# Performance work log

Hardware: AMD Instinct MI355X
Metric: run time of the kernel (lower is better)

Reference implementation:

```python
import jax, jax.numpy as jnp
import numpy as np

N_AGENTS = 3
OBS_DIM = 30
ACT_DIM = 9
HIDDEN = 128
HEADS = 4
HEAD_DIM = HIDDEN // HEADS
BATCH = 131072
NEG_SLOPE = 0.01
MASK_VAL = -1e10


def _leaky(x):
    return jnp.where(x >= 0, x, NEG_SLOPE * x)


def setup_inputs() -> dict:
    key = jax.random.key(0)
    ks = jax.random.split(key, 20)

    def init(k, shape, fan_in):
        return jax.random.normal(k, shape, dtype=jnp.float32) / np.sqrt(fan_in)

    inp = {
        "observations": jax.random.normal(ks[0], (BATCH, N_AGENTS, OBS_DIM), dtype=jnp.float32),
        "actions": jax.random.uniform(ks[1], (BATCH, N_AGENTS, ACT_DIM), dtype=jnp.float32),
        # per-agent embed weights, stacked over agents: [N, in, out] (already transposed vs torch)
        "W_o": init(ks[2], (N_AGENTS, OBS_DIM, HIDDEN), OBS_DIM),
        "b_o": jnp.zeros((N_AGENTS, HIDDEN), dtype=jnp.float32),
        "W_oa": init(ks[3], (N_AGENTS, OBS_DIM + ACT_DIM, HIDDEN), OBS_DIM + ACT_DIM),
        "b_oa": jnp.zeros((N_AGENTS, HIDDEN), dtype=jnp.float32),
        # shared attention projections: [in, out]
        "Wq": init(ks[4], (HIDDEN, HIDDEN), HIDDEN),
        "bq": jnp.zeros((HIDDEN,), dtype=jnp.float32),
        "Wk": init(ks[5], (HIDDEN, HIDDEN), HIDDEN),
        "bk": jnp.zeros((HIDDEN,), dtype=jnp.float32),
        "Wv": init(ks[6], (HIDDEN, HIDDEN), HIDDEN),
        "bv": jnp.zeros((HIDDEN,), dtype=jnp.float32),
        # per-agent critic MLP: Linear(2H->H) + LeakyReLU + Linear(H->A)
        "Wc1": init(ks[7], (N_AGENTS, 2 * HIDDEN, HIDDEN), 2 * HIDDEN),
        "bc1": jnp.zeros((N_AGENTS, HIDDEN), dtype=jnp.float32),
        "Wc2": init(ks[8], (N_AGENTS, HIDDEN, ACT_DIM), HIDDEN),
        "bc2": jnp.zeros((N_AGENTS, ACT_DIM), dtype=jnp.float32),
    }
    return inp


def reference(observations, actions, W_o, b_o, W_oa, b_oa, Wq, bq, Wk, bk, Wv, bv, Wc1, bc1, Wc2, bc2):
    B, N, _ = observations.shape

    # per-agent embeds as a single batched GEMM over the agent axis
    o_emb = _leaky(jnp.einsum('bnd,ndh->bnh', observations, W_o) + b_o)          # [B,N,H]
    oa = jnp.concatenate([observations, actions], axis=-1)                        # [B,N,O+A]
    oa_emb = _leaky(jnp.einsum('bnd,ndh->bnh', oa, W_oa) + b_oa)                  # [B,N,H]

    # shared Q/K/V projections, split heads -> [B, heads, N, head_dim]
    def heads(x):
        return x.reshape(B, N, HEADS, HEAD_DIM).transpose(0, 2, 1, 3)

    Q = heads(o_emb @ Wq + bq)
    K = heads(oa_emb @ Wk + bk)
    V = heads(oa_emb @ Wv + bv)

    scores = jnp.einsum('bhnd,bhmd->bhnm', Q, K) / np.sqrt(HEAD_DIM).astype(np.float32)
    mask = jnp.where(jnp.eye(N, dtype=bool), jnp.float32(MASK_VAL), 0.0)          # diag masked
    attn = jax.nn.softmax(scores + mask, axis=-1)
    attn_out = jnp.einsum('bhnm,bhmd->bhnd', attn, V)
    attn_out = attn_out.transpose(0, 2, 1, 3).reshape(B, N, HIDDEN)               # [B,N,H]

    # per-agent critics, again batched over the agent axis
    c_in = jnp.concatenate([o_emb, attn_out], axis=-1)                            # [B,N,2H]
    h = _leaky(jnp.einsum('bnd,ndh->bnh', c_in, Wc1) + bc1)
    q_values = jnp.einsum('bnh,nha->bna', h, Wc2) + bc2                           # [B,N,A]
    return q_values
```

## Files before the change

kernel.cpp:

```cpp
#include <hip/hip_runtime.h>
#include <stdint.h>

typedef unsigned short u16;
typedef unsigned int u32;
typedef __attribute__((ext_vector_type(8))) short short8;
typedef __attribute__((ext_vector_type(4))) float floatx4;

#define BATCH   131072
#define NA      3
#define OBS     30
#define ACTD    9
#define HID     128
#define HEADS   4
#define HD      32
#define MB      16
#define ROWS    (MB*NA)
#define LDC     136
#define LDOA    72
#define QSCALE  0.17677669529663687f

#define OFF_WO    0
#define OFF_WOA   12288
#define OFF_WQ    36864
#define OFF_WK    53248
#define OFF_WV    69632
#define OFF_WC1   86016
#define OFF_WC2   184320
#define PRE_TOTAL 190464

__device__ __forceinline__ u16 f2bf(float f) {
    union { float f; u32 u; } v; v.f = f;
    return (u16)((v.u + 0x8000u) >> 16);
}
__device__ __forceinline__ u32 pk_bf16(float a, float b) {
    union { float f; u32 u; } x, y; x.f = a; y.f = b;
    return ((x.u + 0x8000u) >> 16) | ((y.u + 0x8000u) & 0xffff0000u);
}
__device__ __forceinline__ float lo16f(u32 w) { union { u32 u; float f; } v; v.u = w << 16; return v.f; }
__device__ __forceinline__ float hi16f(u32 w) { union { u32 u; float f; } v; v.u = w & 0xffff0000u; return v.f; }
__device__ __forceinline__ float leaky(float x) { return x >= 0.f ? x : 0.01f * x; }

__global__ void prepack_kernel(const float* __restrict__ Wo,  const float* __restrict__ Woa,
                               const float* __restrict__ Wq,  const float* __restrict__ Wk,
                               const float* __restrict__ Wv,  const float* __restrict__ Wc1,
                               const float* __restrict__ Wc2, u16* __restrict__ out) {
    int i = blockIdx.x * blockDim.x + threadIdx.x;
    if (i >= PRE_TOTAL) return;
    const float* src; int K, KT, perA, base, Nsrc, Nlim; float scl = 1.f;
    if (i < OFF_WOA)      { src = Wo;  K = 30;  KT = 1; perA = 4096;  base = OFF_WO;  Nsrc = 128; Nlim = 128; }
    else if (i < OFF_WQ)  { src = Woa; K = 39;  KT = 2; perA = 8192;  base = OFF_WOA; Nsrc = 128; Nlim = 128; }
    else if (i < OFF_WK)  { src = Wq;  K = 128; KT = 4; perA = 16384; base = OFF_WQ;  Nsrc = 128; Nlim = 128; scl = QSCALE; }
    else if (i < OFF_WV)  { src = Wk;  K = 128; KT = 4; perA = 16384; base = OFF_WK;  Nsrc = 128; Nlim = 128; }
    else if (i < OFF_WC1) { src = Wv;  K = 128; KT = 4; perA = 16384; base = OFF_WV;  Nsrc = 128; Nlim = 128; }
    else if (i < OFF_WC2) { src = Wc1; K = 256; KT = 8; perA = 32768; base = OFF_WC1; Nsrc = 128; Nlim = 128; }
    else                  { src = Wc2; K = 128; KT = 4; perA = 2048;  base = OFF_WC2; Nsrc = 9;   Nlim = 9;   }
    int j = i - base;
    int agent = j / perA;
    int r = j - agent * perA;
    int e = r & 7, lane = (r >> 3) & 63, fk = r >> 9;
    int kt = fk % KT, nt = fk / KT;
    int n = nt * 16 + (lane & 15);
    int k = kt * 32 + (lane >> 4) * 8 + e;
    u16 v = 0;
    if (k < K && n < Nlim) v = f2bf(src[(agent * K + k) * Nsrc + n] * scl);
    out[i] = v;
}

__global__ __launch_bounds__(256, 3) void fused_kernel(
    const float* __restrict__ obs, const float* __restrict__ act,
    const float* __restrict__ b_o, const float* __restrict__ b_oa,
    const float* __restrict__ bq,  const float* __restrict__ bk_, const float* __restrict__ bv,
    const float* __restrict__ bc1, const float* __restrict__ bc2,
    const u16* __restrict__ pre, float* __restrict__ out)
{
    __shared__ __align__(16) u16 s_mem[4 * ROWS * LDC];
    __shared__ float2 s_probs[MB * HEADS * NA];
    u16* s_oemb  = s_mem;
    u16* s_oaemb = s_mem + ROWS * LDC;
    u16* s_bufA  = s_mem + 2 * ROWS * LDC;
    u16* s_bufB  = s_mem + 3 * ROWS * LDC;

    const int tid  = threadIdx.x;
    const int wave = tid >> 6, lane = tid & 63;
    const int l15  = lane & 15, quad = lane >> 4;
    const int b0   = blockIdx.x * MB;
    const short8* preV = (const short8*)pre;

    for (int g = tid; g < ROWS * 15; g += 256) {
        int r = g / 15, s = g - r * 15;
        int n = r / MB, bl = r - n * MB;
        const float* src = &obs[((b0 + bl) * NA + n) * OBS + 2 * s];
        *(u32*)&s_bufA[n * (MB * LDOA) + bl * LDOA + 2 * s] = pk_bf16(src[0], src[1]);
    }
    for (int g = tid; g < ROWS * 5; g += 256) {
        int r = g / 5, s = g - r * 5;
        int n = r / MB, bl = r - n * MB;
        const float* src = &act[((b0 + bl) * NA + n) * ACTD + 2 * s];
        float v0 = src[0], v1 = (s < 4) ? src[1] : 0.f;
        *(u32*)&s_bufA[n * (MB * LDOA) + bl * LDOA + 30 + 2 * s] = pk_bf16(v0, v1);
    }
    for (int g = tid; g < ROWS * 12; g += 256) {
        int r = g / 12, s = g - r * 12;
        int n = r / MB, bl = r - n * MB;
        *(u32*)&s_bufA[n * (MB * LDOA) + bl * LDOA + 40 + 2 * s] = 0;
    }
    __syncthreads();

    for (int sj = wave; sj < 12; sj += 4) {
        int osel = sj / 6;
        int rem = sj % 6, agent = rem >> 1, nh = rem & 1;
        int KTn = osel ? 2 : 1;
        const float* bias = osel ? b_oa : b_o;
        int preBase = osel ? (OFF_WOA / 8 + agent * 1024) : (OFF_WO / 8 + agent * 512);
        floatx4 acc[4] = {};
        for (int kt = 0; kt < KTn; kt++) {
            short8 a = *(const short8*)&s_bufA[agent * (MB * LDOA) + l15 * LDOA + kt * 32 + quad * 8];
            for (int n4 = 0; n4 < 4; n4++) {
                int nt = nh * 4 + n4;
                short8 b = preV[preBase + (nt * KTn + kt) * 64 + lane];
                acc[n4] = __builtin_amdgcn_mfma_f32_16x16x32_bf16(a, b, acc[n4], 0, 0, 0);
            }
        }
        u16* dst = osel ? s_oaemb : s_oemb;
        for (int n4 = 0; n4 < 4; n4++) {
            int col = (nh * 4 + n4) * 16 + l15;
            float bb = bias[agent * HID + col];
            for (int rg = 0; rg < 4; rg++) {
                int m = quad * 4 + rg;
                dst[(m * NA + agent) * LDC + col] = f2bf(leaky(acc[n4][rg] + bb));
            }
        }
    }
    __syncthreads();

    for (int sj = wave; sj < 12; sj += 4) {
        int proj = sj / 6;
        int rem = sj % 6, mt = rem >> 1, nh = rem & 1;
        const u16* A = proj ? s_oaemb : s_oemb;
        int preBase = (proj ? OFF_WK : OFF_WQ) / 8;
        const float* bias = proj ? bk_ : bq;
        float bscl = proj ? 1.f : QSCALE;
        floatx4 acc[4] = {};
        for (int kt = 0; kt < 4; kt++) {
            short8 a = *(const short8*)&A[(mt * 16 + l15) * LDC + kt * 32 + quad * 8];
            for (int n4 = 0; n4 < 4; n4++) {
                int nt = nh * 4 + n4;
                short8 b = preV[preBase + (nt * 4 + kt) * 64 + lane];
                acc[n4] = __builtin_amdgcn_mfma_f32_16x16x32_bf16(a, b, acc[n4], 0, 0, 0);
            }
        }
        u16* dst = proj ? s_bufB : s_bufA;
        for (int n4 = 0; n4 < 4; n4++) {
            int col = (nh * 4 + n4) * 16 + l15;
            float bb = bias[col] * bscl;
            for (int rg = 0; rg < 4; rg++) {
                int m = mt * 16 + quad * 4 + rg;
                dst[m * LDC + col] = f2bf(acc[n4][rg] + bb);
            }
        }
    }
    __syncthreads();

    if (tid < MB * HEADS * NA) {
        int e = tid / (HEADS * NA), r = tid - e * HEADS * NA, h = r / NA, n = r - h * NA;
        int m0 = (n == 0) ? 1 : 0;
        int m1 = (n == 2) ? 1 : 2;
        const uint4* qp = (const uint4*)&s_bufA[(e * NA + n) * LDC + h * HD];
        const uint4* kp0 = (const uint4*)&s_bufB[(e * NA + m0) * LDC + h * HD];
        const uint4* kp1 = (const uint4*)&s_bufB[(e * NA + m1) * LDC + h * HD];
        float s0 = 0.f, s1 = 0.f;
        for (int c = 0; c < 4; c++) {
            uint4 qw = qp[c], aw = kp0[c], bw = kp1[c];
            u32 qv[4] = {qw.x, qw.y, qw.z, qw.w};
            u32 av[4] = {aw.x, aw.y, aw.z, aw.w};
            u32 bv_[4] = {bw.x, bw.y, bw.z, bw.w};
            for (int j = 0; j < 4; j++) {
                float ql = lo16f(qv[j]), qh = hi16f(qv[j]);
                s0 += ql * lo16f(av[j]) + qh * hi16f(av[j]);
                s1 += ql * lo16f(bv_[j]) + qh * hi16f(bv_[j]);
            }
        }
        float mx = fmaxf(s0, s1);
        float p0 = __expf(s0 - mx), p1 = __expf(s1 - mx);
        float inv = 1.f / (p0 + p1);
        s_probs[(e * HEADS + h) * NA + n] = make_float2(p0 * inv, p1 * inv);
    }
    __syncthreads();

    for (int sj = wave; sj < 12; sj += 4) {
        int mt = sj >> 2, np = sj & 3;
        floatx4 acc[2] = {};
        for (int kt = 0; kt < 4; kt++) {
            short8 a = *(const short8*)&s_oaemb[(mt * 16 + l15) * LDC + kt * 32 + quad * 8];
            for (int n2 = 0; n2 < 2; n2++) {
                int nt = np * 2 + n2;
                short8 b = preV[OFF_WV / 8 + (nt * 4 + kt) * 64 + lane];
                acc[n2] = __builtin_amdgcn_mfma_f32_16x16x32_bf16(a, b, acc[n2], 0, 0, 0);
            }
        }
        for (int n2 = 0; n2 < 2; n2++) {
            int col = (np * 2 + n2) * 16 + l15;
            float bb = bv[col];
            for (int rg = 0; rg < 4; rg++) {
                int m = mt * 16 + quad * 4 + rg;
                s_bufA[m * LDC + col] = f2bf(acc[n2][rg] + bb);
            }
        }
    }
    __syncthreads();

    if (tid < MB * HEADS * NA) {
        int e = tid / (HEADS * NA), r = tid - e * HEADS * NA, h = r / NA, n = r - h * NA;
        int m0 = (n == 0) ? 1 : 0;
        int m1 = (n == 2) ? 1 : 2;
        float2 p = s_probs[(e * HEADS + h) * NA + n];
        const uint4* v0p = (const uint4*)&s_bufA[(e * NA + m0) * LDC + h * HD];
        const uint4* v1p = (const uint4*)&s_bufA[(e * NA + m1) * LDC + h * HD];
        uint4* dst = (uint4*)&s_oaemb[(e * NA + n) * LDC + h * HD];
        for (int c = 0; c < 4; c++) {
            uint4 aw = v0p[c], bw = v1p[c], ow;
            u32 av[4] = {aw.x, aw.y, aw.z, aw.w};
            u32 bv_[4] = {bw.x, bw.y, bw.z, bw.w};
            u32 ov[4];
            for (int j = 0; j < 4; j++) {
                float lo = p.x * lo16f(av[j]) + p.y * lo16f(bv_[j]);
                float hi = p.x * hi16f(av[j]) + p.y * hi16f(bv_[j]);
                ov[j] = pk_bf16(lo, hi);
            }
            ow.x = ov[0]; ow.y = ov[1]; ow.z = ov[2]; ow.w = ov[3];
            dst[c] = ow;
        }
    }
    __syncthreads();

    for (int sj = wave; sj < 12; sj += 4) {
        int agent = sj >> 2, nq = sj & 3;
        floatx4 acc[2] = {};
        for (int kt = 0; kt < 8; kt++) {
            const u16* A = (kt < 4) ? s_oemb : s_oaemb;
            int kk = (kt & 3) * 32 + quad * 8;
            short8 a = *(const short8*)&A[(l15 * NA + agent) * LDC + kk];
            for (int n2 = 0; n2 < 2; n2++) {
                int nt = nq * 2 + n2;
                short8 b = preV[OFF_WC1 / 8 + agent * 4096 + (nt * 8 + kt) * 64 + lane];
                acc[n2] = __builtin_amdgcn_mfma_f32_16x16x32_bf16(a, b, acc[n2], 0, 0, 0);
            }
        }
        for (int n2 = 0; n2 < 2; n2++) {
            int col = (nq * 2 + n2) * 16 + l15;
            float bb = bc1[agent * HID + col];
            for (int rg = 0; rg < 4; rg++) {
                int m = quad * 4 + rg;
                s_bufB[(m * NA + agent) * LDC + col] = f2bf(leaky(acc[n2][rg] + bb));
            }
        }
    }
    __syncthreads();

    for (int sj = wave; sj < NA; sj += 4) {
        int agent = sj;
        floatx4 acc = {};
        for (int kt = 0; kt < 4; kt++) {
            short8 a = *(const short8*)&s_bufB[(l15 * NA + agent) * LDC + kt * 32 + quad * 8];
            short8 b = preV[OFF_WC2 / 8 + agent * 256 + kt * 64 + lane];
            acc = __builtin_amdgcn_mfma_f32_16x16x32_bf16(a, b, acc, 0, 0, 0);
        }
        int col = l15;
        if (col < ACTD) {
            float bb = bc2[agent * ACTD + col];
            for (int rg = 0; rg < 4; rg++) {
                int m = quad * 4 + rg;
                out[((b0 + m) * NA + agent) * ACTD + col] = acc[rg] + bb;
            }
        }
    }
}

extern "C" void kernel_launch(void* const* d_in, const int* in_sizes, int n_in,
                              void* d_out, int out_size, void* d_ws, size_t ws_size,
                              hipStream_t stream) {
    const float* obs = (const float*)d_in[0];
    const float* act = (const float*)d_in[1];
    const float* Wo  = (const float*)d_in[2];
    const float* bo  = (const float*)d_in[3];
    const float* Woa = (const float*)d_in[4];
    const float* boa = (const float*)d_in[5];
    const float* Wq  = (const float*)d_in[6];
    const float* bq  = (const float*)d_in[7];
    const float* Wk  = (const float*)d_in[8];
    const float* bk  = (const float*)d_in[9];
    const float* Wv  = (const float*)d_in[10];
    const float* bv  = (const float*)d_in[11];
    const float* Wc1 = (const float*)d_in[12];
    const float* bc1 = (const float*)d_in[13];
    const float* Wc2 = (const float*)d_in[14];
    const float* bc2 = (const float*)d_in[15];
    u16* pre = (u16*)d_ws;

    prepack_kernel<<<(PRE_TOTAL + 255) / 256, 256, 0, stream>>>(Wo, Woa, Wq, Wk, Wv, Wc1, Wc2, pre);
    fused_kernel<<<BATCH / MB, 256, 0, stream>>>(obs, act, bo, boa, bq, bk, bv, bc1, bc2, pre,
                                                 (float*)d_out);
}
```

Before: 290.7 us.

## Load inputs straight into MFMA fragments, keep weight fragments in registers, vectorize stores

Drops the shared-memory staging pass for observations and actions, along with its barrier. Each wave now builds its bf16 MFMA input fragments directly from global memory. The MFMA operands are swapped so weights feed the A slot and activations the B slot, which gives each lane 4 contiguous output columns and lets stores become packed 64-bit writes with float4 bias loads. The Q/K and V projections now assign each wave a fixed column slice, load its weight fragments into registers once and reuse them across the three row tiles, at the cost of more VGPRs and possibly lower occupancy.

```diff
diff --git a/kernel.cpp b/kernel.cpp
--- a/kernel.cpp
+++ b/kernel.cpp
@@ -16,7 +16,6 @@
 #define MB      16
 #define ROWS    (MB*NA)
 #define LDC     136
-#define LDOA    72
 #define QSCALE  0.17677669529663687f
 
 #define OFF_WO    0
@@ -27,6 +26,8 @@
 #define OFF_WC1   86016
 #define OFF_WC2   184320
 #define PRE_TOTAL 190464
+
+union S8 { short8 s; u32 w[4]; };
 
 __device__ __forceinline__ u16 f2bf(float f) {
     union { float f; u32 u; } v; v.f = f;
@@ -86,76 +87,91 @@
     const int b0   = blockIdx.x * MB;
     const short8* preV = (const short8*)pre;
 
-    for (int g = tid; g < ROWS * 15; g += 256) {
-        int r = g / 15, s = g - r * 15;
-        int n = r / MB, bl = r - n * MB;
-        const float* src = &obs[((b0 + bl) * NA + n) * OBS + 2 * s];
-        *(u32*)&s_bufA[n * (MB * LDOA) + bl * LDOA + 2 * s] = pk_bf16(src[0], src[1]);
-    }
-    for (int g = tid; g < ROWS * 5; g += 256) {
-        int r = g / 5, s = g - r * 5;
-        int n = r / MB, bl = r - n * MB;
-        const float* src = &act[((b0 + bl) * NA + n) * ACTD + 2 * s];
-        float v0 = src[0], v1 = (s < 4) ? src[1] : 0.f;
-        *(u32*)&s_bufA[n * (MB * LDOA) + bl * LDOA + 30 + 2 * s] = pk_bf16(v0, v1);
-    }
-    for (int g = tid; g < ROWS * 12; g += 256) {
-        int r = g / 12, s = g - r * 12;
-        int n = r / MB, bl = r - n * MB;
-        *(u32*)&s_bufA[n * (MB * LDOA) + bl * LDOA + 40 + 2 * s] = 0;
-    }
-    __syncthreads();
-
     for (int sj = wave; sj < 12; sj += 4) {
-        int osel = sj / 6;
+        int oa = sj / 6;
         int rem = sj % 6, agent = rem >> 1, nh = rem & 1;
-        int KTn = osel ? 2 : 1;
-        const float* bias = osel ? b_oa : b_o;
-        int preBase = osel ? (OFF_WOA / 8 + agent * 1024) : (OFF_WO / 8 + agent * 512);
+        const float* obs_row = obs + ((size_t)(b0 + l15) * NA + agent) * OBS;
+        const float* act_row = act + ((size_t)(b0 + l15) * NA + agent) * ACTD;
+        float a0 = oa ? act_row[0] : 0.f;
+        float a1 = oa ? act_row[1] : 0.f;
+        S8 f0;
+        #pragma unroll
+        for (int p = 0; p < 4; p++) {
+            int k = quad * 8 + 2 * p;
+            bool inobs = k < 30;
+            float2 ov = *(const float2*)(obs_row + (inobs ? k : 0));
+            float va = inobs ? ov.x : a0;
+            float vb = inobs ? ov.y : a1;
+            f0.w[p] = pk_bf16(va, vb);
+        }
+        S8 f1;
+        if (oa) {
+            #pragma unroll
+            for (int p = 0; p < 4; p++) {
+                int j0 = 2 * p;
+                float va = (quad == 0 && j0 < 7) ? act_row[2 + j0] : 0.f;
+                float vb = (quad == 0 && j0 + 1 < 7) ? act_row[3 + j0] : 0.f;
+                f1.w[p] = pk_bf16(va, vb);
+            }
+        }
+        int KT = oa ? 2 : 1;
+        int preBase = oa ? (OFF_WOA / 8 + agent * 1024) : (OFF_WO / 8 + agent * 512);
         floatx4 acc[4] = {};
-        for (int kt = 0; kt < KTn; kt++) {
-            short8 a = *(const short8*)&s_bufA[agent * (MB * LDOA) + l15 * LDOA + kt * 32 + quad * 8];
-            for (int n4 = 0; n4 < 4; n4++) {
-                int nt = nh * 4 + n4;
-                short8 b = preV[preBase + (nt * KTn + kt) * 64 + lane];
-                acc[n4] = __builtin_amdgcn_mfma_f32_16x16x32_bf16(a, b, acc[n4], 0, 0, 0);
-            }
-        }
-        u16* dst = osel ? s_oaemb : s_oemb;
+        #pragma unroll
         for (int n4 = 0; n4 < 4; n4++) {
-            int col = (nh * 4 + n4) * 16 + l15;
-            float bb = bias[agent * HID + col];
-            for (int rg = 0; rg < 4; rg++) {
-                int m = quad * 4 + rg;
-                dst[(m * NA + agent) * LDC + col] = f2bf(leaky(acc[n4][rg] + bb));
-            }
-        }
-    }
-    __syncthreads();
-
-    for (int sj = wave; sj < 12; sj += 4) {
-        int proj = sj / 6;
-        int rem = sj % 6, mt = rem >> 1, nh = rem & 1;
-        const u16* A = proj ? s_oaemb : s_oemb;
+            int nt = nh * 4 + n4;
+            acc[n4] = __builtin_amdgcn_mfma_f32_16x16x32_bf16(preV[preBase + (nt * KT + 0) * 64 + lane], f0.s, acc[n4], 0, 0, 0);
+            if (oa)
+                acc[n4] = __builtin_amdgcn_mfma_f32_16x16x32_bf16(preV[preBase + (nt * KT + 1) * 64 + lane], f1.s, acc[n4], 0, 0, 0);
+        }
+        u16* dst = oa ? s_oaemb : s_oemb;
+        const float* bias = (oa ? b_oa : b_o) + agent * HID;
+        int r = l15 * NA + agent;
+        #pragma unroll
+        for (int n4 = 0; n4 < 4; n4++) {
+            int nb = (nh * 4 + n4) * 16 + quad * 4;
+            float4 bb = *(const float4*)&bias[nb];
+            uint2 w;
+            w.x = pk_bf16(leaky(acc[n4][0] + bb.x), leaky(acc[n4][1] + bb.y));
+            w.y = pk_bf16(leaky(acc[n4][2] + bb.z), leaky(acc[n4][3] + bb.w));
+            *(uint2*)&dst[r * LDC + nb] = w;
+        }
+    }
+    __syncthreads();
+
+    {
+        int proj = wave >> 1, nh = wave & 1;
+        const u16* Abuf = proj ? s_oaemb : s_oemb;
         int preBase = (proj ? OFF_WK : OFF_WQ) / 8;
+        u16* dst = proj ? s_bufB : s_bufA;
         const float* bias = proj ? bk_ : bq;
         float bscl = proj ? 1.f : QSCALE;
-        floatx4 acc[4] = {};
-        for (int kt = 0; kt < 4; kt++) {
-            short8 a = *(const short8*)&A[(mt * 16 + l15) * LDC + kt * 32 + quad * 8];
+        short8 wf[16];
+        #pragma unroll
+        for (int n4 = 0; n4 < 4; n4++)
+            #pragma unroll
+            for (int kt = 0; kt < 4; kt++)
+                wf[n4 * 4 + kt] = preV[preBase + ((nh * 4 + n4) * 4 + kt) * 64 + lane];
+        for (int mt = 0; mt < 3; mt++) {
+            short8 xa[4];
+            #pragma unroll
+            for (int kt = 0; kt < 4; kt++)
+                xa[kt] = *(const short8*)&Abuf[(mt * 16 + l15) * LDC + kt * 32 + quad * 8];
+            floatx4 acc[4] = {};
+            #pragma unroll
+            for (int n4 = 0; n4 < 4; n4++)
+                #pragma unroll
+                for (int kt = 0; kt < 4; kt++)
+                    acc[n4] = __builtin_amdgcn_mfma_f32_16x16x32_bf16(wf[n4 * 4 + kt], xa[kt], acc[n4], 0, 0, 0);
+            int r = mt * 16 + l15;
+            #pragma unroll
             for (int n4 = 0; n4 < 4; n4++) {
-                int nt = nh * 4 + n4;
-                short8 b = preV[preBase + (nt * 4 + kt) * 64 + lane];
-                acc[n4] = __builtin_amdgcn_mfma_f32_16x16x32_bf16(a, b, acc[n4], 0, 0, 0);
-            }
-        }
-        u16* dst = proj ? s_bufB : s_bufA;
-        for (int n4 = 0; n4 < 4; n4++) {
-            int col = (nh * 4 + n4) * 16 + l15;
-            float bb = bias[col] * bscl;
-            for (int rg = 0; rg < 4; rg++) {
-                int m = mt * 16 + quad * 4 + rg;
-                dst[m * LDC + col] = f2bf(acc[n4][rg] + bb);
+                int nb = (nh * 4 + n4) * 16 + quad * 4;
+                float4 bb = *(const float4*)&bias[nb];
+                uint2 w;
+                w.x = pk_bf16(acc[n4][0] + bb.x * bscl, acc[n4][1] + bb.y * bscl);
+                w.y = pk_bf16(acc[n4][2] + bb.z * bscl, acc[n4][3] + bb.w * bscl);
+                *(uint2*)&dst[r * LDC + nb] = w;
             }
         }
     }
@@ -169,11 +185,13 @@
         const uint4* kp0 = (const uint4*)&s_bufB[(e * NA + m0) * LDC + h * HD];
         const uint4* kp1 = (const uint4*)&s_bufB[(e * NA + m1) * LDC + h * HD];
         float s0 = 0.f, s1 = 0.f;
+        #pragma unroll
         for (int c = 0; c < 4; c++) {
             uint4 qw = qp[c], aw = kp0[c], bw = kp1[c];
             u32 qv[4] = {qw.x, qw.y, qw.z, qw.w};
             u32 av[4] = {aw.x, aw.y, aw.z, aw.w};
             u32 bv_[4] = {bw.x, bw.y, bw.z, bw.w};
+            #pragma unroll
             for (int j = 0; j < 4; j++) {
                 float ql = lo16f(qv[j]), qh = hi16f(qv[j]);
                 s0 += ql * lo16f(av[j]) + qh * hi16f(av[j]);
@@ -187,23 +205,34 @@
     }
     __syncthreads();
 
-    for (int sj = wave; sj < 12; sj += 4) {
-        int mt = sj >> 2, np = sj & 3;
-        floatx4 acc[2] = {};
-        for (int kt = 0; kt < 4; kt++) {
-            short8 a = *(const short8*)&s_oaemb[(mt * 16 + l15) * LDC + kt * 32 + quad * 8];
+    {
+        int np = wave;
+        short8 wf[8];
+        #pragma unroll
+        for (int n2 = 0; n2 < 2; n2++)
+            #pragma unroll
+            for (int kt = 0; kt < 4; kt++)
+                wf[n2 * 4 + kt] = preV[OFF_WV / 8 + ((np * 2 + n2) * 4 + kt) * 64 + lane];
+        for (int mt = 0; mt < 3; mt++) {
+            short8 xa[4];
+            #pragma unroll
+            for (int kt = 0; kt < 4; kt++)
+                xa[kt] = *(const short8*)&s_oaemb[(mt * 16 + l15) * LDC + kt * 32 + quad * 8];
+            floatx4 acc[2] = {};
+            #pragma unroll
+            for (int n2 = 0; n2 < 2; n2++)
+                #pragma unroll
+                for (int kt = 0; kt < 4; kt++)
+                    acc[n2] = __builtin_amdgcn_mfma_f32_16x16x32_bf16(wf[n2 * 4 + kt], xa[kt], acc[n2], 0, 0, 0);
+            int r = mt * 16 + l15;
+            #pragma unroll
             for (int n2 = 0; n2 < 2; n2++) {
-                int nt = np * 2 + n2;
-                short8 b = preV[OFF_WV / 8 + (nt * 4 + kt) * 64 + lane];
-                acc[n2] = __builtin_amdgcn_mfma_f32_16x16x32_bf16(a, b, acc[n2], 0, 0, 0);
-            }
-        }
-        for (int n2 = 0; n2 < 2; n2++) {
-            int col = (np * 2 + n2) * 16 + l15;
-            float bb = bv[col];
-            for (int rg = 0; rg < 4; rg++) {
-                int m = mt * 16 + quad * 4 + rg;
-                s_bufA[m * LDC + col] = f2bf(acc[n2][rg] + bb);
+                int nb = (np * 2 + n2) * 16 + quad * 4;
+                float4 bb = *(const float4*)&bv[nb];
+                uint2 w;
+                w.x = pk_bf16(acc[n2][0] + bb.x, acc[n2][1] + bb.y);
+                w.y = pk_bf16(acc[n2][2] + bb.z, acc[n2][3] + bb.w);
+                *(uint2*)&s_bufA[r * LDC + nb] = w;
             }
         }
     }
@@ -217,11 +246,13 @@
         const uint4* v0p = (const uint4*)&s_bufA[(e * NA + m0) * LDC + h * HD];
         const uint4* v1p = (const uint4*)&s_bufA[(e * NA + m1) * LDC + h * HD];
         uint4* dst = (uint4*)&s_oaemb[(e * NA + n) * LDC + h * HD];
+        #pragma unroll
         for (int c = 0; c < 4; c++) {
             uint4 aw = v0p[c], bw = v1p[c], ow;
             u32 av[4] = {aw.x, aw.y, aw.z, aw.w};
             u32 bv_[4] = {bw.x, bw.y, bw.z, bw.w};
             u32 ov[4];
+            #pragma unroll
             for (int j = 0; j < 4; j++) {
                 float lo = p.x * lo16f(av[j]) + p.y * lo16f(bv_[j]);
                 float hi = p.x * hi16f(av[j]) + p.y * hi16f(bv_[j]);
@@ -235,43 +266,47 @@
 
     for (int sj = wave; sj < 12; sj += 4) {
         int agent = sj >> 2, nq = sj & 3;
-        floatx4 acc[2] = {};
+        int r = l15 * NA + agent;
+        short8 xa[8];
+        #pragma unroll
         for (int kt = 0; kt < 8; kt++) {
             const u16* A = (kt < 4) ? s_oemb : s_oaemb;
-            int kk = (kt & 3) * 32 + quad * 8;
-            short8 a = *(const short8*)&A[(l15 * NA + agent) * LDC + kk];
-            for (int n2 = 0; n2 < 2; n2++) {
-                int nt = nq * 2 + n2;
-                short8 b = preV[OFF_WC1 / 8 + agent * 4096 + (nt * 8 + kt) * 64 + lane];
-                acc[n2] = __builtin_amdgcn_mfma_f32_16x16x32_bf16(a, b, acc[n2], 0, 0, 0);
-            }
-        }
+            xa[kt] = *(const short8*)&A[r * LDC + (kt & 3) * 32 + quad * 8];
+        }
+        floatx4 acc[2] = {};
+        #pragma unroll
+        for (int n2 = 0; n2 < 2; n2++)
+            #pragma unroll
+            for (int kt = 0; kt < 8; kt++) {
+                short8 wfr = preV[OFF_WC1 / 8 + agent * 4096 + ((nq * 2 + n2) * 8 + kt) * 64 + lane];
+                acc[n2] = __builtin_amdgcn_mfma_f32_16x16x32_bf16(wfr, xa[kt], acc[n2], 0, 0, 0);
+            }
+        #pragma unroll
         for (int n2 = 0; n2 < 2; n2++) {
-            int col = (nq * 2 + n2) * 16 + l15;
-            float bb = bc1[agent * HID + col];
-            for (int rg = 0; rg < 4; rg++) {
-                int m = quad * 4 + rg;
-                s_bufB[(m * NA + agent) * LDC + col] = f2bf(leaky(acc[n2][rg] + bb));
-            }
-        }
-    }
-    __syncthreads();
-
-    for (int sj = wave; sj < NA; sj += 4) {
-        int agent = sj;
+            int nb = (nq * 2 + n2) * 16 + quad * 4;
+            float4 bb = *(const float4*)&bc1[agent * HID + nb];
+            uint2 w;
+            w.x = pk_bf16(leaky(acc[n2][0] + bb.x), leaky(acc[n2][1] + bb.y));
+            w.y = pk_bf16(leaky(acc[n2][2] + bb.z), leaky(acc[n2][3] + bb.w));
+            *(uint2*)&s_bufB[r * LDC + nb] = w;
+        }
+    }
+    __syncthreads();
+
+    if (wave < NA) {
+        int agent = wave;
+        int r = l15 * NA + agent;
         floatx4 acc = {};
+        #pragma unroll
         for (int kt = 0; kt < 4; kt++) {
-            short8 a = *(const short8*)&s_bufB[(l15 * NA + agent) * LDC + kt * 32 + quad * 8];
-            short8 b = preV[OFF_WC2 / 8 + agent * 256 + kt * 64 + lane];
-            acc = __builtin_amdgcn_mfma_f32_16x16x32_bf16(a, b, acc, 0, 0, 0);
-        }
-        int col = l15;
-        if (col < ACTD) {
-            float bb = bc2[agent * ACTD + col];
-            for (int rg = 0; rg < 4; rg++) {
-                int m = quad * 4 + rg;
-                out[((b0 + m) * NA + agent) * ACTD + col] = acc[rg] + bb;
-            }
+            short8 xa = *(const short8*)&s_bufB[r * LDC + kt * 32 + quad * 8];
+            acc = __builtin_amdgcn_mfma_f32_16x16x32_bf16(preV[OFF_WC2 / 8 + agent * 256 + kt * 64 + lane], xa, acc, 0, 0, 0);
+        }
+        #pragma unroll
+        for (int rg = 0; rg < 4; rg++) {
+            int n = quad * 4 + rg;
+            if (n < ACTD)
+                out[((size_t)(b0 + l15) * NA + agent) * ACTD + n] = acc[rg] + bc2[agent * ACTD + n];
         }
     }
 }
```

New measurement: 314.5 us. +8.2%, slower.
